# Kernel tuning notes

Hardware: AMD Instinct MI355X
Metric: run time of the kernel (lower is better)

## Reference

```python
import jax, jax.numpy as jnp
import numpy as np

POOL_SIZES = [(5, 10), (3, 6), (2, 4)]
P_VALUE = 1e-8
EVAL_T = 0.03


def _pool_up(k, p0, p1):
    # avg_pool2d with kernel=stride=(H/p0, W/p1), padding 0 (exact divisibility),
    # followed by repeat_interleave upsampling back to (B,H,W,D).
    B, H, W, D = k.shape
    kh, kw = H // p0, W // p1
    pooled = k.reshape(B, p0, kh, p1, kw, D).mean(axis=(2, 4))  # (B,p0,p1,D)
    up = jnp.broadcast_to(pooled[:, :, None, :, None, :], (B, p0, kh, p1, kw, D))
    return up.reshape(B, H, W, D)


def setup_inputs() -> dict:
    key = jax.random.key(0)
    ks = jax.random.split(key, 7)
    B, H, W, D = 64, 30, 60, 64
    x = jax.random.normal(ks[0], (B, H, W, D), dtype=jnp.float32)
    qk_w = jax.random.normal(ks[1], (2 * D, D), dtype=jnp.float32) * 0.02
    qk_b = jax.random.normal(ks[2], (2 * D,), dtype=jnp.float32) * 0.02
    score_w = jax.random.normal(ks[3], (1, 3), dtype=jnp.float32) * 0.5
    score_b = jax.random.normal(ks[4], (1,), dtype=jnp.float32) * 0.5
    noise_x = jax.random.uniform(ks[5], (B, H * W, 1), dtype=jnp.float32)
    noise_r = jax.random.uniform(ks[6], (B, H * W, 1), dtype=jnp.float32)
    return {"x": x, "qk_w": qk_w, "qk_b": qk_b, "score_w": score_w,
            "score_b": score_b, "noise_x": noise_x, "noise_r": noise_r}


def reference(x, qk_w, qk_b, score_w, score_b, noise_x, noise_r):
    B, H, W, D = x.shape
    scale = D ** (-0.5)
    qk = x @ qk_w.T + qk_b                      # (B,H,W,2D)
    q, k = qk[..., :D], qk[..., D:]             # (B,H,W,D)
    # attn[:,0,1:] only uses row 0 (original q) vs pooled k columns 1..3.
    scores = jnp.stack(
        [jnp.sum(q * _pool_up(k, p0, p1), axis=-1) for (p0, p1) in POOL_SIZES],
        axis=-1) * scale                        # (B,H,W,3)
    attn = scores @ score_w.T + score_b         # (B,H,W,1)
    attn = attn.reshape(B, H * W, 1)
    attn_soft = jax.nn.sigmoid(attn)
    # gumbel-sigmoid (eval mode, T = 0.03)
    gx = jnp.log(attn_soft + P_VALUE)
    gr = jnp.log(1.0 - attn_soft + P_VALUE)
    nx = -jnp.log(-jnp.log(noise_x + P_VALUE) + P_VALUE)
    nr = -jnp.log(-jnp.log(noise_r + P_VALUE) + P_VALUE)
    gx = (gx + nx) / (EVAL_T + P_VALUE)
    gr = (gr + nr) / (EVAL_T + P_VALUE)
    logits = jnp.concatenate([gx, gr], axis=-1)  # (B,HW,2)
    mask = jax.nn.softmax(logits, axis=-1)[..., 0:1]  # (B,HW,1)
    return mask
```

## Files before the change

kernel.cpp:

```cpp
#include <hip/hip_runtime.h>
#include <math.h>

#define BB 64
#define HH 30
#define WW 60
#define DD 64
#define NPIX 1800

__constant__ int c_colband[WW] = {0,0,0,0,0,0, 1,1,1,1, 2,2, 3,3,3, 4,4,4, 5,5, 6,6,6,6, 7,7,7,7,7,7,
                                  8,8,8,8,8,8, 9,9,9,9, 10,10, 11,11,11, 12,12,12, 13,13, 14,14,14,14, 15,15,15,15,15,15};
__constant__ int c_band_start[8] = {0,6,10,12,15,18,20,24};
__constant__ int c_band_cnt[8]   = {6,4,2,3,3,2,4,6};
__constant__ int c_first[20] = {0,1,3,5,7,8,9,11,13,15, 0,2,6,8,10,14, 0,4,8,12};
__constant__ int c_cnt[20]   = {1,2,2,2,1,1,2,2,2,1,   2,4,2,2,4,2,   4,4,4,4};
__constant__ int c_s0col[16] = {0,1,1,2,2,3,3,4,5,6,6,7,7,8,8,9};
__constant__ int c_s1col[16] = {0,0,1,1,1,1,2,2,3,3,4,4,4,4,5,5};
__constant__ int c_s0bf[5] = {0,1,3,5,7};
__constant__ int c_s0bc[5] = {1,2,2,2,1};
__constant__ int c_s1bf[3] = {0,2,6};
__constant__ int c_s1bc[3] = {2,4,2};
__constant__ int c_s2bf[2] = {0,4};

__global__ __launch_bounds__(256) void k1_pool_E(
    const float* __restrict__ x, const float* __restrict__ qk_w,
    const float* __restrict__ qk_b, float* __restrict__ bandsums,
    float* __restrict__ ET_ws, float* __restrict__ u_ws,
    float* __restrict__ v_ws, float* __restrict__ s_ws)
{
    const int t = threadIdx.x;

    if (blockIdx.x >= 512) {
        const int e = blockIdx.x - 512;
        if (t < 64) {
            float acc = 0.f;
#pragma unroll 8
            for (int jj = 0; jj < 64; ++jj)
                acc += qk_w[jj * 64 + t] * qk_w[(64 + e) * 64 + jj];
            acc = 0.f;
#pragma unroll 8
            for (int jj = 0; jj < 64; ++jj)
                acc += qk_w[jj * 64 + t] * qk_w[(64 + jj) * 64 + e];
            ET_ws[e * 64 + t] = acc;
        } else if (e == 0 && t >= 64 && t < 128) {
            const int d = t - 64;
            float acc = 0.f;
            for (int jj = 0; jj < 64; ++jj) acc += qk_w[jj * 64 + d] * qk_b[64 + jj];
            u_ws[d] = acc;
        } else if (e == 0 && t >= 128 && t < 192) {
            const int e2 = t - 128;
            float acc = 0.f;
            for (int jj = 0; jj < 64; ++jj) acc += qk_w[(64 + jj) * 64 + e2] * qk_b[jj];
            v_ws[e2] = acc;
        } else if (e == 0 && t == 192) {
            float acc = 0.f;
            for (int jj = 0; jj < 64; ++jj) acc += qk_b[jj] * qk_b[64 + jj];
            s_ws[0] = acc;
        }
        return;
    }

    __shared__ float pools[16 * 64];
    const int b = blockIdx.x >> 3;
    const int band = blockIdx.x & 7;
    const int j = t & 63;
    const int g = t >> 6;
    const int h0 = c_band_start[band];
    const int nr = c_band_cnt[band];

    float A0 = 0.f, A1 = 0.f, A2 = 0.f, A3 = 0.f;
    for (int r = 0; r < nr; ++r) {
        const float* xrow = x + ((size_t)(b * NPIX + (h0 + r) * WW) + g * 15) * DD;
        float v[15];
#pragma unroll
        for (int i = 0; i < 15; ++i) v[i] = xrow[i * DD + j];
        if ((g & 1) == 0) {
            A0 += ((v[0]+v[1])+(v[2]+v[3]))+(v[4]+v[5]);
            A1 += (v[6]+v[7])+(v[8]+v[9]);
            A2 += v[10]+v[11];
            A3 += (v[12]+v[13])+v[14];
        } else {
            A0 += (v[0]+v[1])+v[2];
            A1 += v[3]+v[4];
            A2 += (v[5]+v[6])+(v[7]+v[8]);
            A3 += ((v[9]+v[10])+(v[11]+v[12]))+(v[13]+v[14]);
        }
    }
    pools[(g * 4 + 0) * 64 + j] = A0;
    pools[(g * 4 + 1) * 64 + j] = A1;
    pools[(g * 4 + 2) * 64 + j] = A2;
    pools[(g * 4 + 3) * 64 + j] = A3;
    __syncthreads();

    float* outp = bandsums + (((size_t)b * 8 + band) * 20) * 64;
    for (int i = t; i < 20 * 64; i += 256) {
        const int c = i >> 6, d = i & 63;
        const int f = c_first[c], n = c_cnt[c];
        float s = 0.f;
        for (int q = 0; q < n; ++q) s += pools[(f + q) * 64 + d];
        outp[i] = s;
    }
}

__global__ __launch_bounds__(256) void k2_mask(
    const float* __restrict__ x, const float* __restrict__ score_w,
    const float* __restrict__ score_b, const float* __restrict__ bandsums,
    const float* __restrict__ ET_ws, const float* __restrict__ u_ws,
    const float* __restrict__ v_ws, const float* __restrict__ s_ws,
    const float* __restrict__ noise_x, const float* __restrict__ noise_r,
    float* __restrict__ out)
{
    __shared__ float ET[64 * 64];
    __shared__ float R[20 * 64];
    __shared__ float XC[16 * 64];
    __shared__ float Gl[16 * 64];
    __shared__ float ul[64], vl[64];
    __shared__ float crow[16];
    __shared__ float attnv[64];

    const int b = blockIdx.x / HH;
    const int h = blockIdx.x % HH;
    const int t = threadIdx.x;
    const int lane = t & 63;
    const int g = t >> 6;

    for (int i = t; i < 4096; i += 256) ET[i] = ET_ws[i];
    if (t < 64) ul[t] = u_ws[t];
    else if (t < 128) vl[t - 64] = v_ws[t - 64];

    const int s0r = h / 6, s1r = h / 10, s2r = h / 15;
    const float* bs = bandsums + (size_t)b * 8 * 20 * 64;
    for (int i = t; i < 20 * 64; i += 256) {
        const int c = i >> 6;
        int f, n;
        if (c < 10)      { f = c_s0bf[s0r]; n = c_s0bc[s0r]; }
        else if (c < 16) { f = c_s1bf[s1r]; n = c_s1bc[s1r]; }
        else             { f = c_s2bf[s2r]; n = 4; }
        float s = 0.f;
        for (int q = 0; q < n; ++q) s += bs[((size_t)(f + q) * 20) * 64 + i];
        R[i] = s;
    }
    __syncthreads();

    const float w0n = score_w[0] * (1.0f / 36.0f);
    const float w1n = score_w[1] * (1.0f / 100.0f);
    const float w2n = score_w[2] * (1.0f / 225.0f);
    for (int i = t; i < 16 * 64; i += 256) {
        const int cb = i >> 6, d = i & 63;
        XC[i] = w0n * R[c_s0col[cb] * 64 + d]
              + w1n * R[(10 + c_s1col[cb]) * 64 + d]
              + w2n * R[(16 + (cb >> 2)) * 64 + d];
    }
    __syncthreads();

    {
        const float wsum = score_w[0] + score_w[1] + score_w[2];
        const float sv = s_ws[0];
        const float sb = score_b[0];
        float xfrag[4], acc[4];
#pragma unroll
        for (int ci = 0; ci < 4; ++ci) {
            xfrag[ci] = XC[(g * 4 + ci) * 64 + lane];
            acc[ci] = 0.f;
        }
#pragma unroll 16
        for (int e = 0; e < 64; ++e) {
            const float ecol = ET[e * 64 + lane];
#pragma unroll
            for (int ci = 0; ci < 4; ++ci)
                acc[ci] += ecol * __shfl(xfrag[ci], e, 64);
        }
#pragma unroll
        for (int ci = 0; ci < 4; ++ci) {
            const int cg = g * 4 + ci;
            Gl[cg * 64 + lane] = 0.125f * (acc[ci] + wsum * ul[lane]);
            float pv = vl[lane] * xfrag[ci];
            pv += __shfl_xor(pv, 1, 64);  pv += __shfl_xor(pv, 2, 64);
            pv += __shfl_xor(pv, 4, 64);  pv += __shfl_xor(pv, 8, 64);
            pv += __shfl_xor(pv, 16, 64); pv += __shfl_xor(pv, 32, 64);
            if (lane == 0) crow[cg] = 0.125f * (pv + wsum * sv) + sb;
        }
    }
    __syncthreads();

    const float4* x4 = (const float4*)(x + (size_t)(b * NPIX + h * WW) * DD);
    const int f = lane & 15;
    const int pg = lane >> 4;
#pragma unroll
    for (int i = 0; i < 4; ++i) {
        const int pl = i * 4 + pg;
        if (pl < 15) {
            const int p = g * 15 + pl;
            const int cb = c_colband[p];
            const float4 xv = x4[p * 16 + f];
            const float4 gv = ((const float4*)Gl)[cb * 16 + f];
            float s = xv.x * gv.x + xv.y * gv.y + xv.z * gv.z + xv.w * gv.w;
            s += __shfl_xor(s, 1, 64);
            s += __shfl_xor(s, 2, 64);
            s += __shfl_xor(s, 4, 64);
            s += __shfl_xor(s, 8, 64);
            if (f == 0) attnv[p] = s + crow[cb];
        }
    }
    __syncthreads();

    if (t < 60) {
        const int pix = b * NPIX + h * WW + t;
        const float a = attnv[t];
        const float sg = 1.0f / (1.0f + expf(-a));
        const float gx = logf(sg + 1e-8f);
        const float gr = logf(1.0f - sg + 1e-8f);
        const float ux = noise_x[pix];
        const float ur = noise_r[pix];
        const float nx = -logf(-logf(ux + 1e-8f) + 1e-8f);
        const float nr = -logf(-logf(ur + 1e-8f) + 1e-8f);
        const float INV_T = 1.0f / (0.03f + 1e-8f);
        const float A = (gx + nx) * INV_T;
        const float Rr = (gr + nr) * INV_T;
        out[pix] = 1.0f / (1.0f + expf(Rr - A));
    }
}

extern "C" void kernel_launch(void* const* d_in, const int* in_sizes, int n_in,
                              void* d_out, int out_size, void* d_ws, size_t ws_size,
                              hipStream_t stream)
{
    const float* x       = (const float*)d_in[0];
    const float* qk_w    = (const float*)d_in[1];
    const float* qk_b    = (const float*)d_in[2];
    const float* score_w = (const float*)d_in[3];
    const float* score_b = (const float*)d_in[4];
    const float* noise_x = (const float*)d_in[5];
    const float* noise_r = (const float*)d_in[6];
    float* out = (float*)d_out;

    float* bandsums = (float*)d_ws;
    float* ET_ws = bandsums + 655360;
    float* u_ws  = ET_ws + 4096;
    float* v_ws  = u_ws + 64;
    float* s_ws  = v_ws + 64;

    k1_pool_E<<<576, 256, 0, stream>>>(x, qk_w, qk_b, bandsums, ET_ws, u_ws, v_ws, s_ws);
    k2_mask<<<BB * HH, 256, 0, stream>>>(x, score_w, score_b, bandsums, ET_ws, u_ws, v_ws, s_ws,
                                         noise_x, noise_r, out);
}
```

Baseline: 128.7 us.

## Process a whole row band per block in mask kernel, reusing G setup

The mask kernel now launches one block per (batch, row band), 512 blocks, instead of one per (batch, row), 1920 blocks. The ET load, region sums and G/crow computation are shared across all rows in the band, so that setup runs less often. The G matvec now holds ET columns in 64 registers and reads XC as broadcast float4 instead of using shuffles, and a dead duplicate loop in k1 is removed. The risks are fewer blocks (less parallelism for the x streaming) and higher register pressure.

```diff
diff --git a/kernel.cpp b/kernel.cpp
--- a/kernel.cpp
+++ b/kernel.cpp
@@ -15,6 +15,8 @@
 __constant__ int c_cnt[20]   = {1,2,2,2,1,1,2,2,2,1,   2,4,2,2,4,2,   4,4,4,4};
 __constant__ int c_s0col[16] = {0,1,1,2,2,3,3,4,5,6,6,7,7,8,8,9};
 __constant__ int c_s1col[16] = {0,0,1,1,1,1,2,2,3,3,4,4,4,4,5,5};
+__constant__ int c_s0row[8] = {0,1,1,2,2,3,3,4};
+__constant__ int c_s1row[8] = {0,0,1,1,1,1,2,2};
 __constant__ int c_s0bf[5] = {0,1,3,5,7};
 __constant__ int c_s0bc[5] = {1,2,2,2,1};
 __constant__ int c_s1bf[3] = {0,2,6};
@@ -33,10 +35,6 @@
         const int e = blockIdx.x - 512;
         if (t < 64) {
             float acc = 0.f;
-#pragma unroll 8
-            for (int jj = 0; jj < 64; ++jj)
-                acc += qk_w[jj * 64 + t] * qk_w[(64 + e) * 64 + jj];
-            acc = 0.f;
 #pragma unroll 8
             for (int jj = 0; jj < 64; ++jj)
                 acc += qk_w[jj * 64 + t] * qk_w[(64 + jj) * 64 + e];
@@ -101,7 +99,7 @@
     }
 }
 
-__global__ __launch_bounds__(256) void k2_mask(
+__global__ __launch_bounds__(256) void k2_G_mask(
     const float* __restrict__ x, const float* __restrict__ score_w,
     const float* __restrict__ score_b, const float* __restrict__ bandsums,
     const float* __restrict__ ET_ws, const float* __restrict__ u_ws,
@@ -109,25 +107,29 @@
     const float* __restrict__ noise_x, const float* __restrict__ noise_r,
     float* __restrict__ out)
 {
-    __shared__ float ET[64 * 64];
+    __shared__ float ETs[4096];
     __shared__ float R[20 * 64];
     __shared__ float XC[16 * 64];
     __shared__ float Gl[16 * 64];
     __shared__ float ul[64], vl[64];
     __shared__ float crow[16];
-    __shared__ float attnv[64];
-
-    const int b = blockIdx.x / HH;
-    const int h = blockIdx.x % HH;
+    __shared__ float attnv[360];
+    __shared__ int cbt[64];
+
+    const int b = blockIdx.x >> 3;
+    const int rb = blockIdx.x & 7;
     const int t = threadIdx.x;
     const int lane = t & 63;
     const int g = t >> 6;
-
-    for (int i = t; i < 4096; i += 256) ET[i] = ET_ws[i];
+    const int h0 = c_band_start[rb];
+    const int nr = c_band_cnt[rb];
+
+    for (int i = t; i < 4096; i += 256) ETs[i] = ET_ws[i];
     if (t < 64) ul[t] = u_ws[t];
     else if (t < 128) vl[t - 64] = v_ws[t - 64];
-
-    const int s0r = h / 6, s1r = h / 10, s2r = h / 15;
+    if (t < 60) cbt[t] = c_colband[t];
+
+    const int s0r = c_s0row[rb], s1r = c_s1row[rb], s2r = rb >> 2;
     const float* bs = bandsums + (size_t)b * 8 * 20 * 64;
     for (int i = t; i < 20 * 64; i += 256) {
         const int c = i >> 6;
@@ -136,7 +138,7 @@
         else if (c < 16) { f = c_s1bf[s1r]; n = c_s1bc[s1r]; }
         else             { f = c_s2bf[s2r]; n = 4; }
         float s = 0.f;
-        for (int q = 0; q < n; ++q) s += bs[((size_t)(f + q) * 20) * 64 + i];
+        for (int q = 0; q < n; ++q) s += bs[(size_t)(f + q) * 20 * 64 + i];
         R[i] = s;
     }
     __syncthreads();
@@ -153,69 +155,74 @@
     __syncthreads();
 
     {
+        float et[64];
+#pragma unroll
+        for (int e = 0; e < 64; ++e) et[e] = ETs[e * 64 + lane];
+
         const float wsum = score_w[0] + score_w[1] + score_w[2];
         const float sv = s_ws[0];
         const float sb = score_b[0];
-        float xfrag[4], acc[4];
+        const float uval = ul[lane];
+        const float vval = vl[lane];
+
 #pragma unroll
         for (int ci = 0; ci < 4; ++ci) {
-            xfrag[ci] = XC[(g * 4 + ci) * 64 + lane];
-            acc[ci] = 0.f;
-        }
-#pragma unroll 16
-        for (int e = 0; e < 64; ++e) {
-            const float ecol = ET[e * 64 + lane];
-#pragma unroll
-            for (int ci = 0; ci < 4; ++ci)
-                acc[ci] += ecol * __shfl(xfrag[ci], e, 64);
-        }
-#pragma unroll
-        for (int ci = 0; ci < 4; ++ci) {
-            const int cg = g * 4 + ci;
-            Gl[cg * 64 + lane] = 0.125f * (acc[ci] + wsum * ul[lane]);
-            float pv = vl[lane] * xfrag[ci];
+            const int cb = g * 4 + ci;
+            const float4* xc4 = (const float4*)(XC + cb * 64);
+            float acc = 0.f;
+#pragma unroll
+            for (int q = 0; q < 16; ++q) {
+                const float4 xv = xc4[q];
+                acc += xv.x * et[4*q] + xv.y * et[4*q+1] + xv.z * et[4*q+2] + xv.w * et[4*q+3];
+            }
+            Gl[cb * 64 + lane] = 0.125f * (acc + wsum * uval);
+
+            float pv = vval * XC[cb * 64 + lane];
             pv += __shfl_xor(pv, 1, 64);  pv += __shfl_xor(pv, 2, 64);
             pv += __shfl_xor(pv, 4, 64);  pv += __shfl_xor(pv, 8, 64);
             pv += __shfl_xor(pv, 16, 64); pv += __shfl_xor(pv, 32, 64);
-            if (lane == 0) crow[cg] = 0.125f * (pv + wsum * sv) + sb;
-        }
-    }
-    __syncthreads();
-
-    const float4* x4 = (const float4*)(x + (size_t)(b * NPIX + h * WW) * DD);
-    const int f = lane & 15;
+            if (lane == 0) crow[cb] = 0.125f * (pv + wsum * sv) + sb;
+        }
+    }
+    __syncthreads();
+
+    const int f16 = lane & 15;
     const int pg = lane >> 4;
-#pragma unroll
-    for (int i = 0; i < 4; ++i) {
-        const int pl = i * 4 + pg;
-        if (pl < 15) {
-            const int p = g * 15 + pl;
-            const int cb = c_colband[p];
-            const float4 xv = x4[p * 16 + f];
-            const float4 gv = ((const float4*)Gl)[cb * 16 + f];
-            float s = xv.x * gv.x + xv.y * gv.y + xv.z * gv.z + xv.w * gv.w;
-            s += __shfl_xor(s, 1, 64);
-            s += __shfl_xor(s, 2, 64);
-            s += __shfl_xor(s, 4, 64);
-            s += __shfl_xor(s, 8, 64);
-            if (f == 0) attnv[p] = s + crow[cb];
-        }
-    }
-    __syncthreads();
-
-    if (t < 60) {
-        const int pix = b * NPIX + h * WW + t;
-        const float a = attnv[t];
+    for (int r = 0; r < nr; ++r) {
+        const float4* x4 = (const float4*)(x + (size_t)(b * NPIX + (h0 + r) * WW) * DD);
+#pragma unroll
+        for (int i = 0; i < 4; ++i) {
+            const int pl = i * 4 + pg;
+            if (pl < 15) {
+                const int p = g * 15 + pl;
+                const int cb = cbt[p];
+                const float4 xv = x4[p * 16 + f16];
+                const float4 gv = ((const float4*)Gl)[cb * 16 + f16];
+                float s = xv.x * gv.x + xv.y * gv.y + xv.z * gv.z + xv.w * gv.w;
+                s += __shfl_xor(s, 1, 64);
+                s += __shfl_xor(s, 2, 64);
+                s += __shfl_xor(s, 4, 64);
+                s += __shfl_xor(s, 8, 64);
+                if (f16 == 0) attnv[r * 60 + p] = s + crow[cb];
+            }
+        }
+    }
+    __syncthreads();
+
+    const int base = b * NPIX + h0 * WW;
+    for (int idx = t; idx < nr * 60; idx += 256) {
+        const int pix = base + idx;
+        const float a = attnv[idx];
         const float sg = 1.0f / (1.0f + expf(-a));
         const float gx = logf(sg + 1e-8f);
         const float gr = logf(1.0f - sg + 1e-8f);
         const float ux = noise_x[pix];
         const float ur = noise_r[pix];
         const float nx = -logf(-logf(ux + 1e-8f) + 1e-8f);
-        const float nr = -logf(-logf(ur + 1e-8f) + 1e-8f);
+        const float nrv = -logf(-logf(ur + 1e-8f) + 1e-8f);
         const float INV_T = 1.0f / (0.03f + 1e-8f);
         const float A = (gx + nx) * INV_T;
-        const float Rr = (gr + nr) * INV_T;
+        const float Rr = (gr + nrv) * INV_T;
         out[pix] = 1.0f / (1.0f + expf(Rr - A));
     }
 }
@@ -240,6 +247,6 @@
     float* s_ws  = v_ws + 64;
 
     k1_pool_E<<<576, 256, 0, stream>>>(x, qk_w, qk_b, bandsums, ET_ws, u_ws, v_ws, s_ws);
-    k2_mask<<<BB * HH, 256, 0, stream>>>(x, score_w, score_b, bandsums, ET_ws, u_ws, v_ws, s_ws,
-                                         noise_x, noise_r, out);
+    k2_G_mask<<<BB * 8, 256, 0, stream>>>(x, score_w, score_b, bandsums, ET_ws, u_ws, v_ws, s_ws,
+                                          noise_x, noise_r, out);
 }
```

After: 109.1 us. 1.18x faster.
